# Optimization experiments

Hardware: AMD Instinct MI355X
Metric: run time of the kernel (lower is better)

The kernel has to match this reference:

```python
import jax, jax.numpy as jnp
import numpy as np

B, D, U = 32768, 256, 256
P0, P1, NC = 128, 64, 1


def setup_inputs() -> dict:
    key = jax.random.key(0)
    ks = jax.random.split(key, 36)
    nrm = lambda k, shp, s=0.05: jax.random.normal(k, shp, jnp.float32) * s
    inp = {
        "x": jax.random.normal(ks[0], (B, D), jnp.float32),
        "click": jax.random.uniform(ks[1], (B, 1), dtype=jnp.float32),
        "h_c": jax.random.normal(ks[2], (B, U), jnp.float32),
        "h_v": jax.random.normal(ks[3], (B, U), jnp.float32),
        "s_c": jax.random.normal(ks[4], (B, U), jnp.float32),
        "s_v": jax.random.normal(ks[5], (B, U), jnp.float32),
        "g_prev": jax.random.randint(ks[6], (B, U), 0, 2).astype(jnp.int32),
        # gate weights: order [f, i, o, g]; x-gates have bias, h-gates do not
        "Wx_c": nrm(ks[7], (4, D, U)), "bx_c": nrm(ks[8], (4, U)), "Wh_c": nrm(ks[9], (4, U, U)),
        "Wx_v": nrm(ks[10], (4, D, U)), "bx_v": nrm(ks[11], (4, U)), "Wh_v": nrm(ks[12], (4, U, U)),
        "W_schat_c": nrm(ks[13], (U, U)), "W_schat_v": nrm(ks[14], (U, U)),
        "W_svhat_v": nrm(ks[15], (U, U)), "W_svhat_c": nrm(ks[16], (U, U)),
        "Wpc0": nrm(ks[17], (U, P0)), "bpc0": nrm(ks[18], (P0,)),
        "Wpc1": nrm(ks[19], (P0, P1)), "bpc1": nrm(ks[20], (P1,)),
        "Wfcc": nrm(ks[21], (P1, NC)), "bfcc": nrm(ks[22], (NC,)),
        "Wpv0": nrm(ks[23], (U, P0)), "bpv0": nrm(ks[24], (P0,)),
        "Wpv1": nrm(ks[25], (P0, P1)), "bpv1": nrm(ks[26], (P1,)),
        "Wfcv": nrm(ks[27], (P1, NC)), "bfcv": nrm(ks[28], (NC,)),
    }
    return inp


def _leaky(x):
    return jnp.where(x > 0, x, 0.3 * x)  # keras LeakyReLU default alpha=0.3


def _mlp(h, W0, b0, W1, b1, Wf, bf):
    a = _leaky(h @ W0 + b0)
    a = _leaky(a @ W1 + b1)
    return jax.nn.sigmoid(a @ Wf + bf)


def reference(x, click, h_c, h_v, s_c, s_v, g_prev,
              Wx_c, bx_c, Wh_c, Wx_v, bx_v, Wh_v,
              W_schat_c, W_schat_v, W_svhat_v, W_svhat_c,
              Wpc0, bpc0, Wpc1, bpc1, Wfcc, bfcc,
              Wpv0, bpv0, Wpv1, bpv1, Wfcv, bfcv):
    gp = g_prev > 0  # [B, U]
    # click branch
    s_c_hat = jnp.where(gp, h_v @ W_schat_v, h_c @ W_schat_c)
    pre_c = (jnp.einsum('bd,kdu->kbu', x, Wx_c) + bx_c[:, None, :]
             + jnp.einsum('bu,kuv->kbv', s_c_hat, Wh_c))  # [4, B, U]
    f_c = jax.nn.sigmoid(pre_c[0]); i_c = jax.nn.sigmoid(pre_c[1])
    o_c = jax.nn.sigmoid(pre_c[2]); g_c = jnp.tanh(pre_c[3])
    s_c_n = i_c * g_c + jnp.where(gp, 0.0, f_c * s_c)
    h_c_n = o_c * jnp.tanh(s_c_n)
    h_c_p = _mlp(h_c_n, Wpc0, bpc0, Wpc1, bpc1, Wfcc, bfcc)  # [B, 1]
    # conversion branch, gated by click label
    gm = click >= 0.5  # [B, 1] broadcasts over U (== tf.tile)
    s_v_hat = h_v @ W_svhat_v + jnp.where(gm, h_c_n @ W_svhat_c, 0.0)
    pre_v = (jnp.einsum('bd,kdu->kbu', x, Wx_v) + bx_v[:, None, :]
             + jnp.einsum('bu,kuv->kbv', s_v_hat, Wh_v))
    f_v = jax.nn.sigmoid(pre_v[0]); i_v = jax.nn.sigmoid(pre_v[1])
    o_v = jax.nn.sigmoid(pre_v[2]); g_v = jnp.tanh(pre_v[3])
    s_v_n = jnp.where(gm, f_v * s_v + i_v * g_v, s_v)
    h_v_n = jnp.where(gm, o_v * jnp.tanh(s_v_n), h_v)
    h_v_p = _mlp(h_v_n, Wpv0, bpv0, Wpv1, bpv1, Wfcv, bfcv) * h_c_p
    g_new = jnp.broadcast_to(gm.astype(jnp.float32), (x.shape[0], U))
    return h_c_p, h_v_p, h_c_n, h_v_n, s_c_n, s_v_n, g_new
```

## Files before the change

kernel.cpp:

```cpp
#include <hip/hip_runtime.h>
#include <hip/hip_bf16.h>
#include <math.h>

typedef __bf16 bf16;
typedef __bf16 bf16x8 __attribute__((ext_vector_type(8)));
typedef float  f32x4  __attribute__((ext_vector_type(4)));

#define NB 32768
#define NU 256

#define MFMA(a,b,c) __builtin_amdgcn_mfma_f32_16x16x32_bf16((a),(b),(c),0,0,0)

static __device__ __forceinline__ float sigf(float x) {
    return __builtin_amdgcn_rcpf(1.0f + __expf(-x));
}
static __device__ __forceinline__ float tanh_(float x) {
    return fmaf(2.0f, sigf(2.0f * x), -1.0f);
}

static __device__ __forceinline__ void ld16(bf16* l, const bf16* g) {
    __builtin_amdgcn_global_load_lds(
        (const __attribute__((address_space(1))) void*)g,
        (__attribute__((address_space(3))) void*)l, 16, 0, 0);
}

static __device__ __forceinline__ bf16x8 frag64(const bf16* buf, int row, int kc) {
    return *reinterpret_cast<const bf16x8*>(buf + row * 64 + ((kc ^ (row & 7)) * 8));
}

__global__ void k_cvt(const float* __restrict__ x, const float* __restrict__ h_v,
                      const float* __restrict__ h_c,
                      bf16* __restrict__ xs, bf16* __restrict__ hv_cat,
                      bf16* __restrict__ hcb)
{
    const int j = blockIdx.y;
    const int gid = blockIdx.x * 256 + threadIdx.x;
    const int row = gid >> 5, col = (gid & 31) * 8;
    const float* src = (j == 0) ? x : (j == 1) ? h_v : h_c;
    bf16* dst; int stride;
    if (j == 0)      { dst = xs;     stride = 512; }
    else if (j == 1) { dst = hv_cat; stride = 512; }
    else             { dst = hcb;    stride = 256; }
    const f32x4* s4 = reinterpret_cast<const f32x4*>(src + row * 256 + col);
    const f32x4 a = s4[0], b = s4[1];
    bf16x8 o;
    o[0] = (bf16)a[0]; o[1] = (bf16)a[1]; o[2] = (bf16)a[2]; o[3] = (bf16)a[3];
    o[4] = (bf16)b[0]; o[5] = (bf16)b[1]; o[6] = (bf16)b[2]; o[7] = (bf16)b[3];
    *reinterpret_cast<bf16x8*>(dst + row * stride + col) = o;
}

__global__ void k_pack(const int* __restrict__ g, unsigned long long* __restrict__ m)
{
    const int tid0 = blockIdx.x * 256 + threadIdx.x;
#pragma unroll
    for (int it = 0; it < 32; ++it) {
        const int i = tid0 + it * (1024 * 256);
        const unsigned long long b = __ballot(g[i] > 0);
        if ((threadIdx.x & 63) == 0) m[i >> 6] = b;
    }
}

struct TrJobs {
    const float* src[24];
    bf16*        dst[24];
    int R[24], C[24], dstr[24];
};

__global__ void k_tr(TrJobs J) {
    __shared__ float tile[32][33];
    const int j = blockIdx.y;
    const int R = J.R[j], C = J.C[j], dstr = J.dstr[j];
    const int tilesC = C >> 5;
    const int tr = blockIdx.x / tilesC, tc = blockIdx.x % tilesC;
    if (tr >= (R >> 5)) return;
    const int r0 = tr * 32, c0 = tc * 32;
    const int tx = threadIdx.x, ty = threadIdx.y;
    const float* src = J.src[j];
    bf16* dst = J.dst[j];
#pragma unroll
    for (int i = 0; i < 4; ++i)
        tile[ty + 8 * i][tx] = src[(r0 + ty + 8 * i) * C + c0 + tx];
    __syncthreads();
#pragma unroll
    for (int i = 0; i < 4; ++i)
        dst[(c0 + ty + 8 * i) * dstr + r0 + tx] = (bf16)tile[tx][ty + 8 * i];
}

__global__ __launch_bounds__(256) void k_schat_t(
    const bf16* __restrict__ hc, const bf16* __restrict__ hvcat,
    const bf16* __restrict__ WTc, const bf16* __restrict__ WTv,
    const unsigned* __restrict__ gmask, bf16* __restrict__ xs)
{
    __shared__ bf16 A1[128 * 64], A2[128 * 64], B1[64 * 64], B2[64 * 64];
    const int tid = threadIdx.x, lane = tid & 63, w = tid >> 6;
    const int lr = lane & 15, hi = lane >> 4;
    const int r0 = blockIdx.x * 128, c0 = blockIdx.y * 64;
    const int wr = w >> 1, wc = w & 1;
    f32x4 acc1[4][2] = {}, acc2[4][2] = {};
    for (int kk = 0; kk < 4; ++kk) {
        const int k0 = kk * 64;
        if (kk) __syncthreads();
#pragma unroll
        for (int p = 0; p < 4; ++p) {
            const int t = tid + p * 256;
            const int row = t >> 3, gs = ((t & 7) ^ (row & 7)) * 8;
            ld16(A1 + t * 8, hc    + (r0 + row) * 256 + k0 + gs);
            ld16(A2 + t * 8, hvcat + (r0 + row) * 512 + k0 + gs);
        }
#pragma unroll
        for (int p = 0; p < 2; ++p) {
            const int t = tid + p * 256;
            const int row = t >> 3, gs = ((t & 7) ^ (row & 7)) * 8;
            ld16(B1 + t * 8, WTc + (c0 + row) * 256 + k0 + gs);
            ld16(B2 + t * 8, WTv + (c0 + row) * 256 + k0 + gs);
        }
        __syncthreads();
#pragma unroll
        for (int ks = 0; ks < 2; ++ks) {
            bf16x8 a1[4], a2[4], b1[2], b2[2];
#pragma unroll
            for (int i = 0; i < 4; ++i) {
                a1[i] = frag64(A1, wr * 64 + i * 16 + lr, ks * 4 + hi);
                a2[i] = frag64(A2, wr * 64 + i * 16 + lr, ks * 4 + hi);
            }
#pragma unroll
            for (int jj = 0; jj < 2; ++jj) {
                b1[jj] = frag64(B1, wc * 32 + jj * 16 + lr, ks * 4 + hi);
                b2[jj] = frag64(B2, wc * 32 + jj * 16 + lr, ks * 4 + hi);
            }
#pragma unroll
            for (int i = 0; i < 4; ++i)
#pragma unroll
                for (int jj = 0; jj < 2; ++jj) {
                    acc1[i][jj] = MFMA(a1[i], b1[jj], acc1[i][jj]);
                    acc2[i][jj] = MFMA(a2[i], b2[jj], acc2[i][jj]);
                }
        }
    }
#pragma unroll
    for (int i = 0; i < 4; ++i)
#pragma unroll
        for (int jj = 0; jj < 2; ++jj)
#pragma unroll
            for (int r = 0; r < 4; ++r) {
                const int row = r0 + wr * 64 + i * 16 + hi * 4 + r;
                const int col = c0 + wc * 32 + jj * 16 + lr;
                const bool gp = (gmask[row * 8 + (col >> 5)] >> (col & 31)) & 1;
                xs[row * 512 + 256 + col] = (bf16)(gp ? acc2[i][jj][r] : acc1[i][jj][r]);
            }
}

__global__ __launch_bounds__(256) void k_svhat_t(
    const bf16* __restrict__ hvcat, const bf16* __restrict__ Wsv,
    bf16* __restrict__ xs)
{
    __shared__ bf16 A[128 * 64], B[128 * 64];
    const int tid = threadIdx.x, lane = tid & 63, w = tid >> 6;
    const int lr = lane & 15, hi = lane >> 4;
    const int r0 = blockIdx.x * 128, c0 = blockIdx.y * 128;
    const int wr = w >> 1, wc = w & 1;
    f32x4 acc[4][4] = {};
    for (int kk = 0; kk < 8; ++kk) {
        const int k0 = kk * 64;
        if (kk) __syncthreads();
#pragma unroll
        for (int p = 0; p < 4; ++p) {
            const int t = tid + p * 256;
            const int row = t >> 3, gs = ((t & 7) ^ (row & 7)) * 8;
            ld16(A + t * 8, hvcat + (r0 + row) * 512 + k0 + gs);
            ld16(B + t * 8, Wsv   + (c0 + row) * 512 + k0 + gs);
        }
        __syncthreads();
#pragma unroll
        for (int ks = 0; ks < 2; ++ks) {
            bf16x8 a[4], b[4];
#pragma unroll
            for (int i = 0; i < 4; ++i) a[i] = frag64(A, wr * 64 + i * 16 + lr, ks * 4 + hi);
#pragma unroll
            for (int jj = 0; jj < 4; ++jj) b[jj] = frag64(B, wc * 64 + jj * 16 + lr, ks * 4 + hi);
#pragma unroll
            for (int i = 0; i < 4; ++i)
#pragma unroll
                for (int jj = 0; jj < 4; ++jj)
                    acc[i][jj] = MFMA(a[i], b[jj], acc[i][jj]);
        }
    }
#pragma unroll
    for (int i = 0; i < 4; ++i)
#pragma unroll
        for (int jj = 0; jj < 4; ++jj)
#pragma unroll
            for (int r = 0; r < 4; ++r) {
                const int row = r0 + wr * 64 + i * 16 + hi * 4 + r;
                const int col = c0 + wc * 64 + jj * 16 + lr;
                xs[row * 512 + 256 + col] = (bf16)acc[i][jj][r];
            }
}

static __device__ __forceinline__ void stageB_gates(
    bf16* dst, const bf16* __restrict__ WgT, int u0, int kk, int tid)
{
#pragma unroll
    for (int p = 0; p < 4; ++p) {
        const int t = tid + p * 256;
        const int row = t >> 3, gs = ((t & 7) ^ (row & 7)) * 8;
        const int g = row >> 5, ul = row & 31;
        ld16(dst + t * 8, WgT + (g * 256 + u0 + ul) * 512 + kk * 64 + gs);
    }
}

__global__ __launch_bounds__(256) void k_gates_t(
    const bf16* __restrict__ xs, const bf16* __restrict__ WgT,
    const float* __restrict__ bx, const float* __restrict__ click,
    const unsigned* __restrict__ gmask, const float* __restrict__ s_prev,
    const float* __restrict__ h_prev,
    float* __restrict__ out_s, float* __restrict__ out_h,
    float* __restrict__ out_g, bf16* __restrict__ hnb,
    bf16* __restrict__ hmask_dst, int mode)
{
    __shared__ bf16 Bs[2][128 * 64];
    const int tid = threadIdx.x, lane = tid & 63, w = tid >> 6;
    const int lr = lane & 15, hi = lane >> 4;
    const int r0 = blockIdx.x * 128, u0 = blockIdx.y * 32;
    const bf16* ap = xs + (size_t)(r0 + w * 32 + lr) * 512 + hi * 8;
    f32x4 acc[2][8] = {};
    stageB_gates(Bs[0], WgT, u0, 0, tid);
    __syncthreads();
#pragma unroll
    for (int kk = 0; kk < 8; ++kk) {
        if (kk < 7) stageB_gates(Bs[(kk + 1) & 1], WgT, u0, kk + 1, tid);
        const bf16* Bc = Bs[kk & 1];
#pragma unroll
        for (int ks = 0; ks < 2; ++ks) {
            bf16x8 a[2], b[8];
#pragma unroll
            for (int i = 0; i < 2; ++i)
                a[i] = *reinterpret_cast<const bf16x8*>(
                    ap + i * 16 * 512 + kk * 64 + ks * 32);
#pragma unroll
            for (int nb = 0; nb < 8; ++nb) b[nb] = frag64(Bc, nb * 16 + lr, ks * 4 + hi);
#pragma unroll
            for (int i = 0; i < 2; ++i)
#pragma unroll
                for (int nb = 0; nb < 8; ++nb)
                    acc[i][nb] = MFMA(a[i], b[nb], acc[i][nb]);
        }
        __syncthreads();
    }
    const int u0b = u0 >> 5;
    float bfv[2], biv[2], bov[2], bgv[2];
#pragma unroll
    for (int uh = 0; uh < 2; ++uh) {
        const int u = u0 + uh * 16 + lr;
        bfv[uh] = bx[u];       biv[uh] = bx[256 + u];
        bov[uh] = bx[512 + u]; bgv[uh] = bx[768 + u];
    }
#pragma unroll
    for (int i = 0; i < 2; ++i)
#pragma unroll
        for (int r = 0; r < 4; ++r) {
            const int row = r0 + w * 32 + i * 16 + hi * 4 + r;
            const float ck = click[row];
            const unsigned mw = (mode == 0) ? gmask[row * 8 + u0b] : 0u;
#pragma unroll
            for (int uh = 0; uh < 2; ++uh) {
                const int u = u0 + uh * 16 + lr;
                const int o = row * 256 + u;
                const float f  = sigf(acc[i][0 + uh][r] + bfv[uh]);
                const float ii = sigf(acc[i][2 + uh][r] + biv[uh]);
                const float oo = sigf(acc[i][4 + uh][r] + bov[uh]);
                const float gg = tanh_(acc[i][6 + uh][r] + bgv[uh]);
                if (mode == 0) {
                    const bool gp = (mw >> (u & 31)) & 1;
                    const float sn = ii * gg + (gp ? 0.0f : f * s_prev[o]);
                    const float hn = oo * tanh_(sn);
                    out_s[o] = sn;
                    out_h[o] = hn;
                    hnb[o]   = (bf16)hn;
                    hmask_dst[row * 512 + 256 + u] =
                        (ck >= 0.5f) ? (bf16)hn : (bf16)0.0f;
                } else {
                    const bool m = ck >= 0.5f;
                    const float sv = s_prev[o];
                    const float sn = m ? (f * sv + ii * gg) : sv;
                    const float hn = m ? (oo * tanh_(sn)) : h_prev[o];
                    out_s[o] = sn;
                    out_h[o] = hn;
                    out_g[o] = m ? 1.0f : 0.0f;
                    hnb[o]   = (bf16)hn;
                }
            }
        }
}

__global__ __launch_bounds__(256) void k_mlp_f(
    const bf16* __restrict__ Hin,
    const bf16* __restrict__ WT0,
    const float* __restrict__ b0,
    const bf16* __restrict__ WT1,
    const float* __restrict__ b1,
    const float* __restrict__ wf,
    const float* __restrict__ bf_,
    const float* __restrict__ scale,
    float* __restrict__ outp)
{
    __shared__ bf16 A[64 * 64], Bb[128 * 64], H1[64 * 128];
    const int tid = threadIdx.x, lane = tid & 63, w = tid >> 6;
    const int lr = lane & 15, hi = lane >> 4;
    const int r0 = blockIdx.x * 64;
    f32x4 acc[8] = {};
    for (int kk = 0; kk < 4; ++kk) {
        const int k0 = kk * 64;
        if (kk) __syncthreads();
#pragma unroll
        for (int p = 0; p < 2; ++p) {
            const int t = tid + p * 256;
            const int row = t >> 3, gs = ((t & 7) ^ (row & 7)) * 8;
            ld16(A + t * 8, Hin + (r0 + row) * 256 + k0 + gs);
        }
#pragma unroll
        for (int p = 0; p < 4; ++p) {
            const int t = tid + p * 256;
            const int row = t >> 3, gs = ((t & 7) ^ (row & 7)) * 8;
            ld16(Bb + t * 8, WT0 + row * 256 + k0 + gs);
        }
        __syncthreads();
#pragma unroll
        for (int ks = 0; ks < 2; ++ks) {
            const bf16x8 a = frag64(A, w * 16 + lr, ks * 4 + hi);
            bf16x8 b[8];
#pragma unroll
            for (int nb = 0; nb < 8; ++nb) b[nb] = frag64(Bb, nb * 16 + lr, ks * 4 + hi);
#pragma unroll
            for (int nb = 0; nb < 8; ++nb) acc[nb] = MFMA(a, b[nb], acc[nb]);
        }
    }
#pragma unroll
    for (int nb = 0; nb < 8; ++nb) {
        const int col = nb * 16 + lr;
        const float bb = b0[col];
#pragma unroll
        for (int r = 0; r < 4; ++r) {
            const int rl = w * 16 + hi * 4 + r;
            float v = acc[nb][r] + bb;
            v = v > 0.0f ? v : 0.3f * v;
            H1[rl * 128 + (((col >> 3) ^ (rl & 7)) * 8) + (col & 7)] = (bf16)v;
        }
    }
    __syncthreads();
    f32x4 acc2[4] = {};
    for (int kk = 0; kk < 2; ++kk) {
#pragma unroll
        for (int p = 0; p < 2; ++p) {
            const int t = tid + p * 256;
            const int row = t >> 3, gs = ((t & 7) ^ (row & 7)) * 8;
            ld16(Bb + t * 8, WT1 + row * 128 + kk * 64 + gs);
        }
        __syncthreads();
#pragma unroll
        for (int ks = 0; ks < 2; ++ks) {
            const int rl = w * 16 + lr;
            const int c = kk * 8 + ks * 4 + hi;
            const bf16x8 a = *reinterpret_cast<const bf16x8*>(
                H1 + rl * 128 + ((c ^ (rl & 7)) * 8));
            bf16x8 b[4];
#pragma unroll
            for (int jj = 0; jj < 4; ++jj) b[jj] = frag64(Bb, jj * 16 + lr, ks * 4 + hi);
#pragma unroll
            for (int jj = 0; jj < 4; ++jj) acc2[jj] = MFMA(a, b[jj], acc2[jj]);
        }
        __syncthreads();
    }
    float b1v[4], wfv[4];
#pragma unroll
    for (int jj = 0; jj < 4; ++jj) {
        b1v[jj] = b1[jj * 16 + lr];
        wfv[jj] = wf[jj * 16 + lr];
    }
    const float bfv = bf_[0];
#pragma unroll
    for (int r = 0; r < 4; ++r) {
        float p = 0.0f;
#pragma unroll
        for (int jj = 0; jj < 4; ++jj) {
            float v = acc2[jj][r] + b1v[jj];
            v = v > 0.0f ? v : 0.3f * v;
            p = fmaf(v, wfv[jj], p);
        }
        p += __shfl_xor(p, 1); p += __shfl_xor(p, 2);
        p += __shfl_xor(p, 4); p += __shfl_xor(p, 8);
        if (lr == 0) {
            const int row = r0 + w * 16 + hi * 4 + r;
            float res = sigf(p + bfv);
            if (scale) res *= scale[row];
            outp[row] = res;
        }
    }
}

extern "C" void kernel_launch(void* const* d_in, const int* in_sizes, int n_in,
                              void* d_out, int out_size, void* d_ws, size_t ws_size,
                              hipStream_t stream)
{
    const float* x         = (const float*)d_in[0];
    const float* click     = (const float*)d_in[1];
    const float* h_c       = (const float*)d_in[2];
    const float* h_v       = (const float*)d_in[3];
    const float* s_c       = (const float*)d_in[4];
    const float* s_v       = (const float*)d_in[5];
    const int*   g_prev    = (const int*)d_in[6];
    const float* Wx_c      = (const float*)d_in[7];
    const float* bx_c      = (const float*)d_in[8];
    const float* Wh_c      = (const float*)d_in[9];
    const float* Wx_v      = (const float*)d_in[10];
    const float* bx_v      = (const float*)d_in[11];
    const float* Wh_v      = (const float*)d_in[12];
    const float* W_schat_c = (const float*)d_in[13];
    const float* W_schat_v = (const float*)d_in[14];
    const float* W_svhat_v = (const float*)d_in[15];
    const float* W_svhat_c = (const float*)d_in[16];
    const float* Wpc0 = (const float*)d_in[17];
    const float* bpc0 = (const float*)d_in[18];
    const float* Wpc1 = (const float*)d_in[19];
    const float* bpc1 = (const float*)d_in[20];
    const float* Wfcc = (const float*)d_in[21];
    const float* bfcc = (const float*)d_in[22];
    const float* Wpv0 = (const float*)d_in[23];
    const float* bpv0 = (const float*)d_in[24];
    const float* Wpv1 = (const float*)d_in[25];
    const float* bpv1 = (const float*)d_in[26];
    const float* Wfcv = (const float*)d_in[27];
    const float* bfcv = (const float*)d_in[28];

    float* out     = (float*)d_out;
    float* out_hcp = out;
    float* out_hvp = out + NB;
    float* out_hcn = out + 2 * NB;
    float* out_hvn = out_hcn + NB * NU;
    float* out_scn = out_hvn + NB * NU;
    float* out_svn = out_scn + NB * NU;
    float* out_gnw = out_svn + NB * NU;

    unsigned long long* gmask64 = (unsigned long long*)d_ws;
    const unsigned* gmask32 = (const unsigned*)d_ws;
    bf16* w = (bf16*)d_ws + 524288;
    bf16* WTc    = w; w += 256 * 256;
    bf16* WTv    = w; w += 256 * 256;
    bf16* Wsv    = w; w += 256 * 512;
    bf16* WT_pc0 = w; w += 128 * 256;
    bf16* WT_pv0 = w; w += 128 * 256;
    bf16* WT_pc1 = w; w += 64 * 128;
    bf16* WT_pv1 = w; w += 64 * 128;
    bf16* WgT_c  = w; w += 4 * 256 * 512;
    bf16* WgT_v  = w; w += 4 * 256 * 512;
    bf16* xs     = w; w += NB * 512;
    bf16* hv_cat = w; w += NB * 512;
    bf16* buf256 = w; w += NB * 256;

    TrJobs J;
    int j = 0;
    J.src[j] = W_schat_c; J.dst[j] = WTc; J.R[j] = 256; J.C[j] = 256; J.dstr[j] = 256; ++j;
    J.src[j] = W_schat_v; J.dst[j] = WTv; J.R[j] = 256; J.C[j] = 256; J.dstr[j] = 256; ++j;
    J.src[j] = W_svhat_v; J.dst[j] = Wsv;       J.R[j] = 256; J.C[j] = 256; J.dstr[j] = 512; ++j;
    J.src[j] = W_svhat_c; J.dst[j] = Wsv + 256; J.R[j] = 256; J.C[j] = 256; J.dstr[j] = 512; ++j;
    J.src[j] = Wpc0; J.dst[j] = WT_pc0; J.R[j] = 256; J.C[j] = 128; J.dstr[j] = 256; ++j;
    J.src[j] = Wpv0; J.dst[j] = WT_pv0; J.R[j] = 256; J.C[j] = 128; J.dstr[j] = 256; ++j;
    J.src[j] = Wpc1; J.dst[j] = WT_pc1; J.R[j] = 128; J.C[j] = 64;  J.dstr[j] = 128; ++j;
    J.src[j] = Wpv1; J.dst[j] = WT_pv1; J.R[j] = 128; J.C[j] = 64;  J.dstr[j] = 128; ++j;
    for (int g = 0; g < 4; ++g) {
        J.src[j] = Wx_c + g * 65536; J.dst[j] = WgT_c + g * 131072;       J.R[j] = 256; J.C[j] = 256; J.dstr[j] = 512; ++j;
        J.src[j] = Wh_c + g * 65536; J.dst[j] = WgT_c + g * 131072 + 256; J.R[j] = 256; J.C[j] = 256; J.dstr[j] = 512; ++j;
    }
    for (int g = 0; g < 4; ++g) {
        J.src[j] = Wx_v + g * 65536; J.dst[j] = WgT_v + g * 131072;       J.R[j] = 256; J.C[j] = 256; J.dstr[j] = 512; ++j;
        J.src[j] = Wh_v + g * 65536; J.dst[j] = WgT_v + g * 131072 + 256; J.R[j] = 256; J.C[j] = 256; J.dstr[j] = 512; ++j;
    }

    k_cvt<<<dim3(4096, 3), 256, 0, stream>>>(x, h_v, h_c, xs, hv_cat, buf256);
    k_pack<<<1024, 256, 0, stream>>>(g_prev, gmask64);
    k_tr<<<dim3(64, 24), dim3(32, 8), 0, stream>>>(J);

    k_schat_t<<<dim3(256, 4), 256, 0, stream>>>(buf256, hv_cat, WTc, WTv, gmask32, xs);
    k_gates_t<<<dim3(256, 8), 256, 0, stream>>>(xs, WgT_c, bx_c, click, gmask32, s_c,
                                                nullptr, out_scn, out_hcn, nullptr,
                                                buf256, hv_cat, 0);
    k_mlp_f<<<512, 256, 0, stream>>>(buf256, WT_pc0, bpc0, WT_pc1, bpc1,
                                     Wfcc, bfcc, nullptr, out_hcp);

    k_svhat_t<<<dim3(256, 2), 256, 0, stream>>>(hv_cat, Wsv, xs);
    k_gates_t<<<dim3(256, 8), 256, 0, stream>>>(xs, WgT_v, bx_v, click, gmask32, s_v,
                                                h_v, out_svn, out_hvn, out_gnw,
                                                buf256, nullptr, 1);
    k_mlp_f<<<512, 256, 0, stream>>>(buf256, WT_pv0, bpv0, WT_pv1, bpv1,
                                     Wfcv, bfcv, out_hcp, out_hvp);
}
```

Baseline: 607.4 us.

## Double-buffer LDS staging in svhat and stage A operand through LDS in gates

The svhat GEMM kernel now double-buffers its A and B tiles in LDS, prefetching the next K slice while the current one is computed, so the per-iteration load-wait-barrier stall is removed. The gates kernel, which read its A operand straight from global memory with direct vector loads, now stages A through swizzled, double-buffered LDS in the same way as B. This overlaps global latency with MFMA work but doubles LDS use per block (64KB in gates), which may lower occupancy.

```diff
diff --git a/kernel.cpp b/kernel.cpp
--- a/kernel.cpp
+++ b/kernel.cpp
@@ -150,40 +150,51 @@
             }
 }
 
+static __device__ __forceinline__ void stage_sv(
+    bf16* Ad, bf16* Bd, const bf16* __restrict__ hvcat,
+    const bf16* __restrict__ Wsv, int r0, int c0, int kk, int tid)
+{
+#pragma unroll
+    for (int p = 0; p < 4; ++p) {
+        const int t = tid + p * 256;
+        const int row = t >> 3, gs = ((t & 7) ^ (row & 7)) * 8;
+        ld16(Ad + t * 8, hvcat + (r0 + row) * 512 + kk * 64 + gs);
+        ld16(Bd + t * 8, Wsv   + (c0 + row) * 512 + kk * 64 + gs);
+    }
+}
+
 __global__ __launch_bounds__(256) void k_svhat_t(
     const bf16* __restrict__ hvcat, const bf16* __restrict__ Wsv,
     bf16* __restrict__ xs)
 {
-    __shared__ bf16 A[128 * 64], B[128 * 64];
+    __shared__ bf16 As[2][128 * 64], Bs[2][128 * 64];
     const int tid = threadIdx.x, lane = tid & 63, w = tid >> 6;
     const int lr = lane & 15, hi = lane >> 4;
     const int r0 = blockIdx.x * 128, c0 = blockIdx.y * 128;
     const int wr = w >> 1, wc = w & 1;
     f32x4 acc[4][4] = {};
+    stage_sv(As[0], Bs[0], hvcat, Wsv, r0, c0, 0, tid);
+    __syncthreads();
+#pragma unroll
     for (int kk = 0; kk < 8; ++kk) {
-        const int k0 = kk * 64;
-        if (kk) __syncthreads();
-#pragma unroll
-        for (int p = 0; p < 4; ++p) {
-            const int t = tid + p * 256;
-            const int row = t >> 3, gs = ((t & 7) ^ (row & 7)) * 8;
-            ld16(A + t * 8, hvcat + (r0 + row) * 512 + k0 + gs);
-            ld16(B + t * 8, Wsv   + (c0 + row) * 512 + k0 + gs);
-        }
-        __syncthreads();
+        if (kk < 7)
+            stage_sv(As[(kk + 1) & 1], Bs[(kk + 1) & 1], hvcat, Wsv, r0, c0, kk + 1, tid);
+        const bf16* Ac = As[kk & 1];
+        const bf16* Bc = Bs[kk & 1];
 #pragma unroll
         for (int ks = 0; ks < 2; ++ks) {
             bf16x8 a[4], b[4];
 #pragma unroll
-            for (int i = 0; i < 4; ++i) a[i] = frag64(A, wr * 64 + i * 16 + lr, ks * 4 + hi);
-#pragma unroll
-            for (int jj = 0; jj < 4; ++jj) b[jj] = frag64(B, wc * 64 + jj * 16 + lr, ks * 4 + hi);
+            for (int i = 0; i < 4; ++i) a[i] = frag64(Ac, wr * 64 + i * 16 + lr, ks * 4 + hi);
+#pragma unroll
+            for (int jj = 0; jj < 4; ++jj) b[jj] = frag64(Bc, wc * 64 + jj * 16 + lr, ks * 4 + hi);
 #pragma unroll
             for (int i = 0; i < 4; ++i)
 #pragma unroll
                 for (int jj = 0; jj < 4; ++jj)
                     acc[i][jj] = MFMA(a[i], b[jj], acc[i][jj]);
         }
+        __syncthreads();
     }
 #pragma unroll
     for (int i = 0; i < 4; ++i)
@@ -195,6 +206,17 @@
                 const int col = c0 + wc * 64 + jj * 16 + lr;
                 xs[row * 512 + 256 + col] = (bf16)acc[i][jj][r];
             }
+}
+
+static __device__ __forceinline__ void stageA_gates(
+    bf16* dst, const bf16* __restrict__ xs, int r0, int kk, int tid)
+{
+#pragma unroll
+    for (int p = 0; p < 4; ++p) {
+        const int t = tid + p * 256;
+        const int row = t >> 3, gs = ((t & 7) ^ (row & 7)) * 8;
+        ld16(dst + t * 8, xs + (r0 + row) * 512 + kk * 64 + gs);
+    }
 }
 
 static __device__ __forceinline__ void stageB_gates(
@@ -218,25 +240,27 @@
     float* __restrict__ out_g, bf16* __restrict__ hnb,
     bf16* __restrict__ hmask_dst, int mode)
 {
-    __shared__ bf16 Bs[2][128 * 64];
+    __shared__ bf16 As[2][128 * 64], Bs[2][128 * 64];
     const int tid = threadIdx.x, lane = tid & 63, w = tid >> 6;
     const int lr = lane & 15, hi = lane >> 4;
     const int r0 = blockIdx.x * 128, u0 = blockIdx.y * 32;
-    const bf16* ap = xs + (size_t)(r0 + w * 32 + lr) * 512 + hi * 8;
     f32x4 acc[2][8] = {};
+    stageA_gates(As[0], xs, r0, 0, tid);
     stageB_gates(Bs[0], WgT, u0, 0, tid);
     __syncthreads();
 #pragma unroll
     for (int kk = 0; kk < 8; ++kk) {
-        if (kk < 7) stageB_gates(Bs[(kk + 1) & 1], WgT, u0, kk + 1, tid);
+        if (kk < 7) {
+            stageA_gates(As[(kk + 1) & 1], xs, r0, kk + 1, tid);
+            stageB_gates(Bs[(kk + 1) & 1], WgT, u0, kk + 1, tid);
+        }
+        const bf16* Ac = As[kk & 1];
         const bf16* Bc = Bs[kk & 1];
 #pragma unroll
         for (int ks = 0; ks < 2; ++ks) {
             bf16x8 a[2], b[8];
 #pragma unroll
-            for (int i = 0; i < 2; ++i)
-                a[i] = *reinterpret_cast<const bf16x8*>(
-                    ap + i * 16 * 512 + kk * 64 + ks * 32);
+            for (int i = 0; i < 2; ++i) a[i] = frag64(Ac, w * 32 + i * 16 + lr, ks * 4 + hi);
 #pragma unroll
             for (int nb = 0; nb < 8; ++nb) b[nb] = frag64(Bc, nb * 16 + lr, ks * 4 + hi);
 #pragma unroll
```

Result: no change. 618.8 us (+1.9%).
